# Optimization experiments

Hardware: AMD Instinct MI355X
Metric: run time of the kernel (lower is better)

Reference implementation:

```python
import jax, jax.numpy as jnp
import numpy as np

EPS = 1e-06  # slot-attention renorm epsilon
LN_EPS = 1e-05  # torch LayerNorm default
NUM_ITERS = 3


def layernorm(x, w, b):
    m = jnp.mean(x, axis=-1, keepdims=True)
    v = jnp.mean((x - m) ** 2, axis=-1, keepdims=True)
    return (x - m) * jax.lax.rsqrt(v + LN_EPS) * w + b


def setup_inputs() -> dict:
    key = jax.random.key(0)
    ks = jax.random.split(key, 16)
    B, N, D = 32, 4096, 512
    S, NS, H = 128, 8, 256
    def lin(k, out_f, in_f):
        return jax.random.normal(k, (out_f, in_f), jnp.float32) * (1.0 / np.sqrt(in_f))
    return {
        "inputs": jax.random.normal(ks[0], (B, N, D), jnp.float32),
        "slots_init": jax.random.normal(ks[1], (B, NS, S), jnp.float32),
        "ln_in_w": jnp.ones((D,), jnp.float32), "ln_in_b": jnp.zeros((D,), jnp.float32),
        "ln_slot_w": jnp.ones((S,), jnp.float32), "ln_slot_b": jnp.zeros((S,), jnp.float32),
        "ln_mlp_w": jnp.ones((S,), jnp.float32), "ln_mlp_b": jnp.zeros((S,), jnp.float32),
        "Wq": lin(ks[2], S, S), "Wk": lin(ks[3], S, D), "Wv": lin(ks[4], S, D),
        "gru_Wih": lin(ks[5], 3 * S, S), "gru_Whh": lin(ks[6], 3 * S, S),
        "gru_bih": jnp.zeros((3 * S,), jnp.float32), "gru_bhh": jnp.zeros((3 * S,), jnp.float32),
        "mlp_W1": lin(ks[7], H, S), "mlp_b1": jnp.zeros((H,), jnp.float32),
        "mlp_W2": lin(ks[8], S, H), "mlp_b2": jnp.zeros((S,), jnp.float32),
        "slots_mu": jax.random.normal(ks[9], (1, 1, S), jnp.float32) * 0.1,
        "slots_log_sigma": jax.random.normal(ks[10], (1, 1, S), jnp.float32) * 0.1,
    }


def gru_cell(x, h, Wih, Whh, bih, bhh):
    # PyTorch GRUCell math. x, h: [BS, S]
    S = h.shape[-1]
    gi = x @ Wih.T + bih
    gh = h @ Whh.T + bhh
    i_r, i_z, i_n = gi[:, :S], gi[:, S:2 * S], gi[:, 2 * S:]
    h_r, h_z, h_n = gh[:, :S], gh[:, S:2 * S], gh[:, 2 * S:]
    r = jax.nn.sigmoid(i_r + h_r)
    z = jax.nn.sigmoid(i_z + h_z)
    n = jnp.tanh(i_n + r * h_n)
    return (1.0 - z) * n + z * h


def reference(inputs, slots_init, ln_in_w, ln_in_b, ln_slot_w, ln_slot_b, ln_mlp_w, ln_mlp_b,
              Wq, Wk, Wv, gru_Wih, gru_Whh, gru_bih, gru_bhh,
              mlp_W1, mlp_b1, mlp_W2, mlp_b2, slots_mu, slots_log_sigma):
    B, N, D = inputs.shape
    NS, S = slots_init.shape[1], slots_init.shape[2]
    x = layernorm(inputs, ln_in_w, ln_in_b)
    k = jnp.einsum('bnd,sd->bns', x, Wk)  # [B,N,S]
    v = jnp.einsum('bnd,sd->bns', x, Wv)
    slots = slots_mu + jnp.exp(slots_log_sigma) * slots_init  # [B,NS,S]
    scale = S ** (-0.5)
    for _ in range(NUM_ITERS):
        slots_prev = slots
        q = jnp.einsum('bmd,sd->bms', layernorm(slots, ln_slot_w, ln_slot_b), Wq)  # [B,NS,S]
        attn_logits = scale * jnp.einsum('bns,bms->bnm', k, q)  # [B,N,NS]
        attn = jax.nn.softmax(attn_logits, axis=-1) + EPS
        attn = attn / jnp.sum(attn, axis=1, keepdims=True)  # normalize over inputs
        updates = jnp.einsum('bnm,bns->bms', attn, v)  # [B,NS,S]
        h = gru_cell(updates.reshape(B * NS, S), slots_prev.reshape(B * NS, S),
                     gru_Wih, gru_Whh, gru_bih, gru_bhh).reshape(B, NS, S)
        mlp_out = jnp.maximum(layernorm(h, ln_mlp_w, ln_mlp_b) @ mlp_W1.T + mlp_b1, 0.0) @ mlp_W2.T + mlp_b2
        slots = h + mlp_out
    return slots
```

## Files before the change

kernel.cpp:

```cpp
#include <hip/hip_runtime.h>

typedef __bf16 v8bf __attribute__((ext_vector_type(8)));
typedef __bf16 v4bf __attribute__((ext_vector_type(4)));
typedef float  v4f  __attribute__((ext_vector_type(4)));
typedef unsigned short u16;

#define LN_EPS_F 1e-5f
#define ATTN_EPS 1e-6f

static constexpr int Bsz = 32;
static constexpr int Nn  = 4096;
static constexpr int Dd  = 512;
static constexpr int Ss  = 128;
static constexpr int NSs = 8;
static constexpr int Hh  = 256;
static constexpr int MROWS = Bsz * Nn;

__global__ __launch_bounds__(256) void k_stats(const float* __restrict__ X,
                                               float2* __restrict__ stats) {
    const int wid  = threadIdx.x >> 6;
    const int lane = threadIdx.x & 63;
    const int row  = blockIdx.x * 4 + wid;
    const float4* xp = reinterpret_cast<const float4*>(X + (size_t)row * Dd) + lane * 2;
    float4 a = xp[0];
    float4 b = xp[1];
    float s  = a.x + a.y + a.z + a.w + b.x + b.y + b.z + b.w;
    float s2 = a.x*a.x + a.y*a.y + a.z*a.z + a.w*a.w
             + b.x*b.x + b.y*b.y + b.z*b.z + b.w*b.w;
#pragma unroll
    for (int off = 32; off > 0; off >>= 1) {
        s  += __shfl_xor(s, off);
        s2 += __shfl_xor(s2, off);
    }
    if (lane == 0) {
        float m = s * (1.0f / Dd);
        float v = s2 * (1.0f / Dd) - m * m;
        stats[row] = make_float2(m, rsqrtf(v + LN_EPS_F));
    }
}

__global__ __launch_bounds__(256) void k_prep(const float* __restrict__ Wk, const float* __restrict__ Wv,
                                              const float* __restrict__ ln_in_w, const float* __restrict__ ln_in_b,
                                              const float* __restrict__ slots_init, const float* __restrict__ mu,
                                              const float* __restrict__ lsig,
                                              u16* __restrict__ Wkvp, float* __restrict__ cb,
                                              float* __restrict__ slots) {
    const int bid = blockIdx.x;
    const int t = threadIdx.x;
    if (bid < 512) {
        int idx = bid * 256 + t;
        int n = idx >> 9, d = idx & 511;
        float w = (n < Ss) ? Wk[n * Dd + d] : Wv[(n - Ss) * Dd + d];
        w *= ln_in_w[d];
        __bf16 bv = (__bf16)w;
        Wkvp[idx] = __builtin_bit_cast(u16, bv);
    } else if (bid < 640) {
        int idx = (bid - 512) * 256 + t;
        int sidx = idx & (Ss - 1);
        slots[idx] = mu[sidx] + expf(lsig[sidx]) * slots_init[idx];
    } else {
        const float* wrow = (t < Ss) ? (Wk + t * Dd) : (Wv + (t - Ss) * Dd);
        float acc = 0.f;
        for (int d = 0; d < Dd; ++d) acc += ln_in_b[d] * wrow[d];
        cb[t] = acc;
    }
}

__global__ __launch_bounds__(256) void k_kvgemm(const float* __restrict__ X,
                                                const float2* __restrict__ stats,
                                                const u16* __restrict__ Wkvp,
                                                const float* __restrict__ cb,
                                                u16* __restrict__ kv) {
    __shared__ __bf16 As[64][72];
    __shared__ __bf16 Bs[256][72];
    const int t    = threadIdx.x;
    const int lane = t & 63;
    const int wid  = t >> 6;
    const size_t m0 = (size_t)blockIdx.x * 64;

    const int ar  = t >> 2;
    const int ac0 = (t & 3) * 16;
    const float2 st = stats[m0 + ar];
    const float* xrow = X + (m0 + ar) * Dd;
    const u16* wrow = Wkvp + t * Dd;

    const v4f vzero = {0.f, 0.f, 0.f, 0.f};
    v4f acc[4][4];
#pragma unroll
    for (int i = 0; i < 4; ++i)
#pragma unroll
        for (int j = 0; j < 4; ++j) acc[i][j] = vzero;

    const int g  = lane >> 4;
    const int lr = lane & 15;

    for (int kb = 0; kb < 8; ++kb) {
#pragma unroll
        for (int j = 0; j < 4; ++j) {
            float4 xv = *reinterpret_cast<const float4*>(xrow + kb * 64 + ac0 + j * 4);
            v4bf wv;
            wv[0] = (__bf16)((xv.x - st.x) * st.y);
            wv[1] = (__bf16)((xv.y - st.x) * st.y);
            wv[2] = (__bf16)((xv.z - st.x) * st.y);
            wv[3] = (__bf16)((xv.w - st.x) * st.y);
            *reinterpret_cast<v4bf*>(&As[ar][ac0 + j * 4]) = wv;
        }
#pragma unroll
        for (int p = 0; p < 8; ++p) {
            uint4 u = *reinterpret_cast<const uint4*>(wrow + kb * 64 + p * 8);
            *reinterpret_cast<uint4*>(&Bs[t][p * 8]) = u;
        }
        __syncthreads();
#pragma unroll
        for (int ks = 0; ks < 2; ++ks) {
            v8bf a[4], b[4];
#pragma unroll
            for (int mi = 0; mi < 4; ++mi)
                a[mi] = *reinterpret_cast<const v8bf*>(&As[mi * 16 + lr][ks * 32 + g * 8]);
#pragma unroll
            for (int ni = 0; ni < 4; ++ni)
                b[ni] = *reinterpret_cast<const v8bf*>(&Bs[wid * 64 + ni * 16 + lr][ks * 32 + g * 8]);
#pragma unroll
            for (int mi = 0; mi < 4; ++mi)
#pragma unroll
                for (int ni = 0; ni < 4; ++ni)
                    acc[mi][ni] = __builtin_amdgcn_mfma_f32_16x16x32_bf16(a[mi], b[ni], acc[mi][ni], 0, 0, 0);
        }
        __syncthreads();
    }
    float cbv[4];
#pragma unroll
    for (int ni = 0; ni < 4; ++ni) cbv[ni] = cb[wid * 64 + ni * 16 + lr];
#pragma unroll
    for (int mi = 0; mi < 4; ++mi)
#pragma unroll
        for (int ni = 0; ni < 4; ++ni)
#pragma unroll
            for (int j = 0; j < 4; ++j) {
                size_t mg = m0 + mi * 16 + g * 4 + j;
                int ng = wid * 64 + ni * 16 + lr;
                __bf16 bv = (__bf16)(acc[mi][ni][j] + cbv[ni]);
                kv[mg * 256 + ng] = __builtin_bit_cast(u16, bv);
            }
}

__global__ __launch_bounds__(128) void k_q(const float* __restrict__ slots,
                                           const float* __restrict__ lnw, const float* __restrict__ lnb,
                                           const float* __restrict__ Wq, float* __restrict__ q) {
    __shared__ float xs[128];
    __shared__ float red[4];
    const int t = threadIdx.x;
    const int bm = blockIdx.x;
    float x = slots[bm * 128 + t];
    float s = x, s2 = x * x;
#pragma unroll
    for (int off = 32; off > 0; off >>= 1) { s += __shfl_xor(s, off); s2 += __shfl_xor(s2, off); }
    const int wid = t >> 6, lane = t & 63;
    if (lane == 0) { red[wid * 2] = s; red[wid * 2 + 1] = s2; }
    __syncthreads();
    float S1 = red[0] + red[2], S2 = red[1] + red[3];
    float m = S1 * (1.f / 128.f);
    float rstd = rsqrtf(S2 * (1.f / 128.f) - m * m + LN_EPS_F);
    xs[t] = (x - m) * rstd * lnw[t] + lnb[t];
    __syncthreads();
    const float* wr = Wq + (size_t)t * 128;
    float acc = 0.f;
#pragma unroll 8
    for (int d = 0; d < 128; d += 4) {
        float4 w = *reinterpret_cast<const float4*>(wr + d);
        acc += w.x * xs[d] + w.y * xs[d + 1] + w.z * xs[d + 2] + w.w * xs[d + 3];
    }
    q[bm * 128 + t] = acc * 0.08838834764831845f;
}

__global__ __launch_bounds__(256) void k_attn(const u16* __restrict__ kv, const float* __restrict__ q,
                                              float* __restrict__ attn, float* __restrict__ colsum_part) {
    __shared__ float qs[8][128];
    __shared__ float colpart[4][8];
    const int b  = blockIdx.y;
    const int ch = blockIdx.x;
    const int t  = threadIdx.x;
    for (int i = t; i < NSs * Ss; i += 256) qs[i >> 7][i & 127] = q[b * (NSs * Ss) + i];
    __syncthreads();
    const int nl   = t >> 1;
    const int half = t & 1;
    const int n    = ch * 128 + nl;
    const u16* krow = kv + ((size_t)(b * Nn + n)) * 256 + half * 64;
    float acc[8] = {0.f, 0.f, 0.f, 0.f, 0.f, 0.f, 0.f, 0.f};
#pragma unroll
    for (int c = 0; c < 8; ++c) {
        v8bf kvv = *reinterpret_cast<const v8bf*>(krow + c * 8);
        float kf[8];
#pragma unroll
        for (int j = 0; j < 8; ++j) kf[j] = (float)kvv[j];
#pragma unroll
        for (int m = 0; m < 8; ++m) {
            const float* qrow = &qs[m][half * 64 + c * 8];
            float aa = 0.f;
#pragma unroll
            for (int j = 0; j < 8; ++j) aa += kf[j] * qrow[j];
            acc[m] += aa;
        }
    }
#pragma unroll
    for (int m = 0; m < 8; ++m) acc[m] += __shfl_xor(acc[m], 1);
    float mx = acc[0];
#pragma unroll
    for (int m = 1; m < 8; ++m) mx = fmaxf(mx, acc[m]);
    float e[8]; float ssum = 0.f;
#pragma unroll
    for (int m = 0; m < 8; ++m) { e[m] = __expf(acc[m] - mx); ssum += e[m]; }
    float inv = 1.0f / ssum;
    float a8[8];
#pragma unroll
    for (int m = 0; m < 8; ++m) a8[m] = e[m] * inv + ATTN_EPS;
    float4 outv = half ? make_float4(a8[4], a8[5], a8[6], a8[7])
                       : make_float4(a8[0], a8[1], a8[2], a8[3]);
    *reinterpret_cast<float4*>(attn + ((size_t)(b * Nn + n)) * 8 + half * 4) = outv;
    const int lane = t & 63, w = t >> 6;
#pragma unroll
    for (int m = 0; m < 8; ++m) {
        float v = a8[m];
#pragma unroll
        for (int off = 32; off > 0; off >>= 1) v += __shfl_xor(v, off);
        if (lane == 0) colpart[w][m] = v * 0.5f;
    }
    __syncthreads();
    if (t < 8)
        colsum_part[(b * 32 + ch) * 8 + t] =
            colpart[0][t] + colpart[1][t] + colpart[2][t] + colpart[3][t];
}

__global__ __launch_bounds__(256) void k_upd(const u16* __restrict__ kv, const float* __restrict__ attn,
                                             float* __restrict__ upd_part) {
    __shared__ float at[128][8];
    __shared__ __bf16 vt[128][128];
    const int b  = blockIdx.y;
    const int ch = blockIdx.x;
    const int t  = threadIdx.x;
    {
        float4 v = *reinterpret_cast<const float4*>(attn + ((size_t)(b * Nn + ch * 128)) * 8 + t * 4);
        *reinterpret_cast<float4*>(&at[t >> 1][(t & 1) * 4]) = v;
    }
#pragma unroll
    for (int p = 0; p < 8; ++p) {
        int r = p * 16 + (t >> 4);
        int c = (t & 15) * 8;
        uint4 u = *reinterpret_cast<const uint4*>(kv + ((size_t)(b * Nn + ch * 128 + r)) * 256 + 128 + c);
        *reinterpret_cast<uint4*>(&vt[r][c]) = u;
    }
    __syncthreads();
    const int m  = t >> 5;
    const int s0 = (t & 31) * 4;
    float a0 = 0.f, a1 = 0.f, a2 = 0.f, a3 = 0.f;
#pragma unroll 4
    for (int n = 0; n < 128; ++n) {
        float a = at[n][m];
        v4bf vv = *reinterpret_cast<const v4bf*>(&vt[n][s0]);
        a0 += a * (float)vv[0];
        a1 += a * (float)vv[1];
        a2 += a * (float)vv[2];
        a3 += a * (float)vv[3];
    }
    *reinterpret_cast<float4*>(upd_part + ((size_t)(b * 32 + ch) * 8 + m) * 128 + s0) =
        make_float4(a0, a1, a2, a3);
}

__global__ __launch_bounds__(128) void k_finish(const float* __restrict__ upd_part,
                                                const float* __restrict__ colsum_part,
                                                const float* __restrict__ slots_in,
                                                const float* __restrict__ Wih, const float* __restrict__ Whh,
                                                const float* __restrict__ bih, const float* __restrict__ bhh,
                                                const float* __restrict__ lnw, const float* __restrict__ lnb,
                                                const float* __restrict__ W1, const float* __restrict__ b1,
                                                const float* __restrict__ W2, const float* __restrict__ b2,
                                                float* __restrict__ slots_out) {
    __shared__ float us[128], sp[128], hnorm[128], act[256];
    __shared__ float red[4];
    __shared__ float csum_sh;
    const int t  = threadIdx.x;
    const int bm = blockIdx.x;
    const int b = bm >> 3, m = bm & 7;
    if (t < 64) {
        float v = (t < 32) ? colsum_part[(b * 32 + t) * 8 + m] : 0.f;
#pragma unroll
        for (int off = 32; off > 0; off >>= 1) v += __shfl_xor(v, off);
        if (t == 0) csum_sh = v;
    }
    float u = 0.f;
    for (int chk = 0; chk < 32; ++chk)
        u += upd_part[((size_t)(b * 32 + chk) * 8 + m) * 128 + t];
    float h0 = slots_in[bm * 128 + t];
    sp[t] = h0;
    __syncthreads();
    u *= (1.0f / csum_sh);
    us[t] = u;
    __syncthreads();
    float gir = bih[t], giz = bih[Ss + t], gin = bih[2 * Ss + t];
    float ghr = bhh[t], ghz = bhh[Ss + t], ghn = bhh[2 * Ss + t];
#pragma unroll 4
    for (int d = 0; d < Ss; d += 4) {
        float u0 = us[d], u1 = us[d + 1], u2 = us[d + 2], u3 = us[d + 3];
        float p0 = sp[d], p1 = sp[d + 1], p2 = sp[d + 2], p3 = sp[d + 3];
        float4 w;
        w = *reinterpret_cast<const float4*>(Wih + (size_t)t * Ss + d);
        gir += w.x * u0 + w.y * u1 + w.z * u2 + w.w * u3;
        w = *reinterpret_cast<const float4*>(Wih + (size_t)(Ss + t) * Ss + d);
        giz += w.x * u0 + w.y * u1 + w.z * u2 + w.w * u3;
        w = *reinterpret_cast<const float4*>(Wih + (size_t)(2 * Ss + t) * Ss + d);
        gin += w.x * u0 + w.y * u1 + w.z * u2 + w.w * u3;
        w = *reinterpret_cast<const float4*>(Whh + (size_t)t * Ss + d);
        ghr += w.x * p0 + w.y * p1 + w.z * p2 + w.w * p3;
        w = *reinterpret_cast<const float4*>(Whh + (size_t)(Ss + t) * Ss + d);
        ghz += w.x * p0 + w.y * p1 + w.z * p2 + w.w * p3;
        w = *reinterpret_cast<const float4*>(Whh + (size_t)(2 * Ss + t) * Ss + d);
        ghn += w.x * p0 + w.y * p1 + w.z * p2 + w.w * p3;
    }
    float r  = 1.f / (1.f + __expf(-(gir + ghr)));
    float z  = 1.f / (1.f + __expf(-(giz + ghz)));
    float nn = tanhf(gin + r * ghn);
    float h  = (1.f - z) * nn + z * h0;
    float s = h, s2 = h * h;
#pragma unroll
    for (int off = 32; off > 0; off >>= 1) { s += __shfl_xor(s, off); s2 += __shfl_xor(s2, off); }
    const int lane = t & 63, w2 = t >> 6;
    if (lane == 0) { red[w2 * 2] = s; red[w2 * 2 + 1] = s2; }
    __syncthreads();
    float S1 = red[0] + red[2], S2 = red[1] + red[3];
    float mean = S1 * (1.f / Ss);
    float rstd = rsqrtf(S2 * (1.f / Ss) - mean * mean + LN_EPS_F);
    hnorm[t] = (h - mean) * rstd * lnw[t] + lnb[t];
    __syncthreads();
    float a1 = b1[t], a2 = b1[Ss + t];
#pragma unroll 4
    for (int d = 0; d < Ss; d += 4) {
        float h0_ = hnorm[d], h1_ = hnorm[d + 1], h2_ = hnorm[d + 2], h3_ = hnorm[d + 3];
        float4 w1v = *reinterpret_cast<const float4*>(W1 + (size_t)t * Ss + d);
        float4 w2v = *reinterpret_cast<const float4*>(W1 + (size_t)(Ss + t) * Ss + d);
        a1 += w1v.x * h0_ + w1v.y * h1_ + w1v.z * h2_ + w1v.w * h3_;
        a2 += w2v.x * h0_ + w2v.y * h1_ + w2v.z * h2_ + w2v.w * h3_;
    }
    act[t] = fmaxf(a1, 0.f);
    act[Ss + t] = fmaxf(a2, 0.f);
    __syncthreads();
    float o = b2[t];
#pragma unroll 4
    for (int j = 0; j < Hh; j += 4) {
        float4 wv = *reinterpret_cast<const float4*>(W2 + (size_t)t * Hh + j);
        o += wv.x * act[j] + wv.y * act[j + 1] + wv.z * act[j + 2] + wv.w * act[j + 3];
    }
    slots_out[bm * 128 + t] = h + o;
}

extern "C" void kernel_launch(void* const* d_in, const int* in_sizes, int n_in,
                              void* d_out, int out_size, void* d_ws, size_t ws_size,
                              hipStream_t stream) {
    const float* X          = (const float*)d_in[0];
    const float* slots_init = (const float*)d_in[1];
    const float* ln_in_w    = (const float*)d_in[2];
    const float* ln_in_b    = (const float*)d_in[3];
    const float* ln_slot_w  = (const float*)d_in[4];
    const float* ln_slot_b  = (const float*)d_in[5];
    const float* ln_mlp_w   = (const float*)d_in[6];
    const float* ln_mlp_b   = (const float*)d_in[7];
    const float* Wq         = (const float*)d_in[8];
    const float* Wk         = (const float*)d_in[9];
    const float* Wv         = (const float*)d_in[10];
    const float* gWih       = (const float*)d_in[11];
    const float* gWhh       = (const float*)d_in[12];
    const float* gbih       = (const float*)d_in[13];
    const float* gbhh       = (const float*)d_in[14];
    const float* W1         = (const float*)d_in[15];
    const float* b1         = (const float*)d_in[16];
    const float* W2         = (const float*)d_in[17];
    const float* b2         = (const float*)d_in[18];
    const float* mu         = (const float*)d_in[19];
    const float* lsig       = (const float*)d_in[20];

    char* p = (char*)d_ws;
    float2* stats       = (float2*)p; p += (size_t)MROWS * sizeof(float2);
    u16*    Wkvp        = (u16*)p;    p += (size_t)256 * 512 * sizeof(u16);
    float*  cb          = (float*)p;  p += 256 * sizeof(float);
    float*  slots       = (float*)p;  p += 32 * 8 * 128 * sizeof(float);
    float*  qbuf        = (float*)p;  p += 32 * 8 * 128 * sizeof(float);
    float*  colsum_part = (float*)p;  p += 32 * 32 * 8 * sizeof(float);
    float*  upd_part    = (float*)p;  p += (size_t)32 * 32 * 8 * 128 * sizeof(float);
    float*  attn        = (float*)p;  p += (size_t)MROWS * 8 * sizeof(float);
    u16*    kv          = (u16*)p;    p += (size_t)MROWS * 256 * sizeof(u16);

    k_stats<<<MROWS / 4, 256, 0, stream>>>(X, stats);
    k_prep<<<641, 256, 0, stream>>>(Wk, Wv, ln_in_w, ln_in_b, slots_init, mu, lsig,
                                    Wkvp, cb, slots);
    k_kvgemm<<<MROWS / 64, 256, 0, stream>>>(X, stats, Wkvp, cb, kv);

    for (int it = 0; it < 3; ++it) {
        k_q<<<256, 128, 0, stream>>>(slots, ln_slot_w, ln_slot_b, Wq, qbuf);
        k_attn<<<dim3(32, 32), 256, 0, stream>>>(kv, qbuf, attn, colsum_part);
        k_upd<<<dim3(32, 32), 256, 0, stream>>>(kv, attn, upd_part);
        k_finish<<<256, 128, 0, stream>>>(upd_part, colsum_part, slots,
                                          gWih, gWhh, gbih, gbhh,
                                          ln_mlp_w, ln_mlp_b, W1, b1, W2, b2,
                                          (it == 2) ? (float*)d_out : slots);
    }
}
```

Before: 370.1 us.

## Fuse LayerNorm stats into KV GEMM, merge attn/update and finish/q kernels

Removes the separate row-stats pass by applying input LayerNorm algebraically after the GEMM, using per-column weight sums and row mean/rstd accumulated while the tile is loaded. The B tile now goes through direct global-to-LDS loads into an XOR-swizzled layout. The attention and update kernels are fused so the attn matrix never goes to global memory, and the q projection is folded into the finish kernel. The aim is to cut a full 256MB read of X plus the attn round-trip and several launches, at the cost of bf16 rounding on raw X before centering, which may lose precision.

```diff
diff --git a/kernel.cpp b/kernel.cpp
--- a/kernel.cpp
+++ b/kernel.cpp
@@ -16,27 +16,10 @@
 static constexpr int Hh  = 256;
 static constexpr int MROWS = Bsz * Nn;
 
-__global__ __launch_bounds__(256) void k_stats(const float* __restrict__ X,
-                                               float2* __restrict__ stats) {
-    const int wid  = threadIdx.x >> 6;
-    const int lane = threadIdx.x & 63;
-    const int row  = blockIdx.x * 4 + wid;
-    const float4* xp = reinterpret_cast<const float4*>(X + (size_t)row * Dd) + lane * 2;
-    float4 a = xp[0];
-    float4 b = xp[1];
-    float s  = a.x + a.y + a.z + a.w + b.x + b.y + b.z + b.w;
-    float s2 = a.x*a.x + a.y*a.y + a.z*a.z + a.w*a.w
-             + b.x*b.x + b.y*b.y + b.z*b.z + b.w*b.w;
-#pragma unroll
-    for (int off = 32; off > 0; off >>= 1) {
-        s  += __shfl_xor(s, off);
-        s2 += __shfl_xor(s2, off);
-    }
-    if (lane == 0) {
-        float m = s * (1.0f / Dd);
-        float v = s2 * (1.0f / Dd) - m * m;
-        stats[row] = make_float2(m, rsqrtf(v + LN_EPS_F));
-    }
+__device__ __forceinline__ void load_lds16(const void* g, void* l) {
+    __builtin_amdgcn_global_load_lds(
+        (const __attribute__((address_space(1))) void*)g,
+        (__attribute__((address_space(3))) void*)l, 16, 0, 0);
 }
 
 __global__ __launch_bounds__(256) void k_prep(const float* __restrict__ Wk, const float* __restrict__ Wv,
@@ -44,7 +27,7 @@
                                               const float* __restrict__ slots_init, const float* __restrict__ mu,
                                               const float* __restrict__ lsig,
                                               u16* __restrict__ Wkvp, float* __restrict__ cb,
-                                              float* __restrict__ slots) {
+                                              float* __restrict__ Scol, float* __restrict__ slots) {
     const int bid = blockIdx.x;
     const int t = threadIdx.x;
     if (bid < 512) {
@@ -60,19 +43,26 @@
         slots[idx] = mu[sidx] + expf(lsig[sidx]) * slots_init[idx];
     } else {
         const float* wrow = (t < Ss) ? (Wk + t * Dd) : (Wv + (t - Ss) * Dd);
-        float acc = 0.f;
-        for (int d = 0; d < Dd; ++d) acc += ln_in_b[d] * wrow[d];
-        cb[t] = acc;
+        float accb = 0.f, accs = 0.f;
+        for (int d = 0; d < Dd; ++d) {
+            float w  = wrow[d];
+            float wb = (float)(__bf16)(w * ln_in_w[d]);
+            accs += wb;
+            accb += ln_in_b[d] * w;
+        }
+        cb[t]   = accb;
+        Scol[t] = accs;
     }
 }
 
 __global__ __launch_bounds__(256) void k_kvgemm(const float* __restrict__ X,
-                                                const float2* __restrict__ stats,
                                                 const u16* __restrict__ Wkvp,
                                                 const float* __restrict__ cb,
+                                                const float* __restrict__ Scol,
                                                 u16* __restrict__ kv) {
     __shared__ __bf16 As[64][72];
-    __shared__ __bf16 Bs[256][72];
+    __shared__ __bf16 Bs[256 * 64];
+    __shared__ float2 stats_sh[64];
     const int t    = threadIdx.x;
     const int lane = t & 63;
     const int wid  = t >> 6;
@@ -80,9 +70,11 @@
 
     const int ar  = t >> 2;
     const int ac0 = (t & 3) * 16;
-    const float2 st = stats[m0 + ar];
     const float* xrow = X + (m0 + ar) * Dd;
-    const u16* wrow = Wkvp + t * Dd;
+
+    const int sub  = lane >> 3;
+    const int scol = ((lane & 7) ^ sub) * 8;
+    const u16* bsrc = Wkvp + (size_t)(wid * 64 + sub) * Dd + scol;
 
     const v4f vzero = {0.f, 0.f, 0.f, 0.f};
     v4f acc[4][4];
@@ -93,22 +85,22 @@
 
     const int g  = lane >> 4;
     const int lr = lane & 15;
+    float s1 = 0.f, s2 = 0.f;
 
     for (int kb = 0; kb < 8; ++kb) {
+#pragma unroll
+        for (int p = 0; p < 8; ++p)
+            load_lds16(bsrc + (size_t)p * 8 * Dd + kb * 64,
+                       &Bs[(wid * 64 + p * 8) * 64]);
 #pragma unroll
         for (int j = 0; j < 4; ++j) {
             float4 xv = *reinterpret_cast<const float4*>(xrow + kb * 64 + ac0 + j * 4);
+            s1 += xv.x + xv.y + xv.z + xv.w;
+            s2 += xv.x * xv.x + xv.y * xv.y + xv.z * xv.z + xv.w * xv.w;
             v4bf wv;
-            wv[0] = (__bf16)((xv.x - st.x) * st.y);
-            wv[1] = (__bf16)((xv.y - st.x) * st.y);
-            wv[2] = (__bf16)((xv.z - st.x) * st.y);
-            wv[3] = (__bf16)((xv.w - st.x) * st.y);
+            wv[0] = (__bf16)xv.x; wv[1] = (__bf16)xv.y;
+            wv[2] = (__bf16)xv.z; wv[3] = (__bf16)xv.w;
             *reinterpret_cast<v4bf*>(&As[ar][ac0 + j * 4]) = wv;
-        }
-#pragma unroll
-        for (int p = 0; p < 8; ++p) {
-            uint4 u = *reinterpret_cast<const uint4*>(wrow + kb * 64 + p * 8);
-            *reinterpret_cast<uint4*>(&Bs[t][p * 8]) = u;
         }
         __syncthreads();
 #pragma unroll
@@ -118,8 +110,11 @@
             for (int mi = 0; mi < 4; ++mi)
                 a[mi] = *reinterpret_cast<const v8bf*>(&As[mi * 16 + lr][ks * 32 + g * 8]);
 #pragma unroll
-            for (int ni = 0; ni < 4; ++ni)
-                b[ni] = *reinterpret_cast<const v8bf*>(&Bs[wid * 64 + ni * 16 + lr][ks * 32 + g * 8]);
+            for (int ni = 0; ni < 4; ++ni) {
+                int r = wid * 64 + ni * 16 + lr;
+                b[ni] = *reinterpret_cast<const v8bf*>(
+                    &Bs[r * 64 + ((ks * 32 + g * 8) ^ ((lr & 7) * 8))]);
+            }
 #pragma unroll
             for (int mi = 0; mi < 4; ++mi)
 #pragma unroll
@@ -128,20 +123,35 @@
         }
         __syncthreads();
     }
-    float cbv[4];
-#pragma unroll
-    for (int ni = 0; ni < 4; ++ni) cbv[ni] = cb[wid * 64 + ni * 16 + lr];
+    s1 += __shfl_xor(s1, 1); s1 += __shfl_xor(s1, 2);
+    s2 += __shfl_xor(s2, 1); s2 += __shfl_xor(s2, 2);
+    if ((t & 3) == 0) {
+        float m = s1 * (1.f / Dd);
+        float v = s2 * (1.f / Dd) - m * m;
+        stats_sh[ar] = make_float2(m, rsqrtf(v + LN_EPS_F));
+    }
+    __syncthreads();
+    float Sn[4], cbv[4];
+#pragma unroll
+    for (int ni = 0; ni < 4; ++ni) {
+        int ng = wid * 64 + ni * 16 + lr;
+        Sn[ni]  = Scol[ng];
+        cbv[ni] = cb[ng];
+    }
 #pragma unroll
     for (int mi = 0; mi < 4; ++mi)
 #pragma unroll
-        for (int ni = 0; ni < 4; ++ni)
-#pragma unroll
-            for (int j = 0; j < 4; ++j) {
-                size_t mg = m0 + mi * 16 + g * 4 + j;
+        for (int j = 0; j < 4; ++j) {
+            float2 st = stats_sh[mi * 16 + g * 4 + j];
+            size_t mg = m0 + mi * 16 + g * 4 + j;
+#pragma unroll
+            for (int ni = 0; ni < 4; ++ni) {
                 int ng = wid * 64 + ni * 16 + lr;
-                __bf16 bv = (__bf16)(acc[mi][ni][j] + cbv[ni]);
+                float val = st.y * (acc[mi][ni][j] - st.x * Sn[ni]) + cbv[ni];
+                __bf16 bv = (__bf16)val;
                 kv[mg * 256 + ng] = __builtin_bit_cast(u16, bv);
             }
+        }
 }
 
 __global__ __launch_bounds__(128) void k_q(const float* __restrict__ slots,
@@ -173,19 +183,31 @@
     q[bm * 128 + t] = acc * 0.08838834764831845f;
 }
 
-__global__ __launch_bounds__(256) void k_attn(const u16* __restrict__ kv, const float* __restrict__ q,
-                                              float* __restrict__ attn, float* __restrict__ colsum_part) {
-    __shared__ float qs[8][128];
+__global__ __launch_bounds__(256) void k_attnupd(const u16* __restrict__ kv, const float* __restrict__ q,
+                                                 float* __restrict__ upd_part, float* __restrict__ colsum_part) {
+    __shared__ float qs[8 * 128];
+    __shared__ float at[128][8];
+    __shared__ __bf16 vt[128][128];
     __shared__ float colpart[4][8];
     const int b  = blockIdx.y;
     const int ch = blockIdx.x;
     const int t  = threadIdx.x;
-    for (int i = t; i < NSs * Ss; i += 256) qs[i >> 7][i & 127] = q[b * (NSs * Ss) + i];
-    __syncthreads();
+    const int lane = t & 63, wv = t >> 6;
+    *reinterpret_cast<float4*>(&qs[t * 4]) = *reinterpret_cast<const float4*>(&q[b * 1024 + t * 4]);
+    __syncthreads();
+    {
+        const int rsub = lane >> 4;
+        const int csub = (lane & 15) * 8;
+#pragma unroll
+        for (int p = 0; p < 8; ++p) {
+            int row = wv * 32 + p * 4;
+            const u16* src = kv + ((size_t)(b * Nn + ch * 128 + row + rsub)) * 256 + 128 + csub;
+            load_lds16(src, &vt[row][0]);
+        }
+    }
     const int nl   = t >> 1;
     const int half = t & 1;
-    const int n    = ch * 128 + nl;
-    const u16* krow = kv + ((size_t)(b * Nn + n)) * 256 + half * 64;
+    const u16* krow = kv + ((size_t)(b * Nn + ch * 128 + nl)) * 256 + half * 64;
     float acc[8] = {0.f, 0.f, 0.f, 0.f, 0.f, 0.f, 0.f, 0.f};
 #pragma unroll
     for (int c = 0; c < 8; ++c) {
@@ -195,7 +217,7 @@
         for (int j = 0; j < 8; ++j) kf[j] = (float)kvv[j];
 #pragma unroll
         for (int m = 0; m < 8; ++m) {
-            const float* qrow = &qs[m][half * 64 + c * 8];
+            const float* qrow = &qs[m * 128 + half * 64 + c * 8];
             float aa = 0.f;
 #pragma unroll
             for (int j = 0; j < 8; ++j) aa += kf[j] * qrow[j];
@@ -214,67 +236,46 @@
     float a8[8];
 #pragma unroll
     for (int m = 0; m < 8; ++m) a8[m] = e[m] * inv + ATTN_EPS;
-    float4 outv = half ? make_float4(a8[4], a8[5], a8[6], a8[7])
-                       : make_float4(a8[0], a8[1], a8[2], a8[3]);
-    *reinterpret_cast<float4*>(attn + ((size_t)(b * Nn + n)) * 8 + half * 4) = outv;
-    const int lane = t & 63, w = t >> 6;
+    *reinterpret_cast<float4*>(&at[nl][half * 4]) =
+        make_float4(a8[half * 4], a8[half * 4 + 1], a8[half * 4 + 2], a8[half * 4 + 3]);
 #pragma unroll
     for (int m = 0; m < 8; ++m) {
         float v = a8[m];
 #pragma unroll
         for (int off = 32; off > 0; off >>= 1) v += __shfl_xor(v, off);
-        if (lane == 0) colpart[w][m] = v * 0.5f;
-    }
-    __syncthreads();
-    if (t < 8)
-        colsum_part[(b * 32 + ch) * 8 + t] =
-            colpart[0][t] + colpart[1][t] + colpart[2][t] + colpart[3][t];
-}
-
-__global__ __launch_bounds__(256) void k_upd(const u16* __restrict__ kv, const float* __restrict__ attn,
-                                             float* __restrict__ upd_part) {
-    __shared__ float at[128][8];
-    __shared__ __bf16 vt[128][128];
-    const int b  = blockIdx.y;
-    const int ch = blockIdx.x;
-    const int t  = threadIdx.x;
-    {
-        float4 v = *reinterpret_cast<const float4*>(attn + ((size_t)(b * Nn + ch * 128)) * 8 + t * 4);
-        *reinterpret_cast<float4*>(&at[t >> 1][(t & 1) * 4]) = v;
-    }
-#pragma unroll
-    for (int p = 0; p < 8; ++p) {
-        int r = p * 16 + (t >> 4);
-        int c = (t & 15) * 8;
-        uint4 u = *reinterpret_cast<const uint4*>(kv + ((size_t)(b * Nn + ch * 128 + r)) * 256 + 128 + c);
-        *reinterpret_cast<uint4*>(&vt[r][c]) = u;
-    }
-    __syncthreads();
-    const int m  = t >> 5;
+        if (lane == 0) colpart[wv][m] = v * 0.5f;
+    }
+    __syncthreads();
+    const int m2 = t >> 5;
     const int s0 = (t & 31) * 4;
     float a0 = 0.f, a1 = 0.f, a2 = 0.f, a3 = 0.f;
 #pragma unroll 4
     for (int n = 0; n < 128; ++n) {
-        float a = at[n][m];
-        v4bf vv = *reinterpret_cast<const v4bf*>(&vt[n][s0]);
-        a0 += a * (float)vv[0];
-        a1 += a * (float)vv[1];
-        a2 += a * (float)vv[2];
-        a3 += a * (float)vv[3];
-    }
-    *reinterpret_cast<float4*>(upd_part + ((size_t)(b * 32 + ch) * 8 + m) * 128 + s0) =
+        float a = at[n][m2];
+        v4bf vvv = *reinterpret_cast<const v4bf*>(&vt[n][s0]);
+        a0 += a * (float)vvv[0];
+        a1 += a * (float)vvv[1];
+        a2 += a * (float)vvv[2];
+        a3 += a * (float)vvv[3];
+    }
+    *reinterpret_cast<float4*>(upd_part + ((size_t)(b * 32 + ch) * 8 + m2) * 128 + s0) =
         make_float4(a0, a1, a2, a3);
-}
-
-__global__ __launch_bounds__(128) void k_finish(const float* __restrict__ upd_part,
-                                                const float* __restrict__ colsum_part,
-                                                const float* __restrict__ slots_in,
-                                                const float* __restrict__ Wih, const float* __restrict__ Whh,
-                                                const float* __restrict__ bih, const float* __restrict__ bhh,
-                                                const float* __restrict__ lnw, const float* __restrict__ lnb,
-                                                const float* __restrict__ W1, const float* __restrict__ b1,
-                                                const float* __restrict__ W2, const float* __restrict__ b2,
-                                                float* __restrict__ slots_out) {
+    if (t < 8)
+        colsum_part[(b * 32 + ch) * 8 + t] =
+            colpart[0][t] + colpart[1][t] + colpart[2][t] + colpart[3][t];
+}
+
+__global__ __launch_bounds__(128) void k_finishq(const float* __restrict__ upd_part,
+                                                 const float* __restrict__ colsum_part,
+                                                 const float* __restrict__ slots_in,
+                                                 const float* __restrict__ Wih, const float* __restrict__ Whh,
+                                                 const float* __restrict__ bih, const float* __restrict__ bhh,
+                                                 const float* __restrict__ lnw, const float* __restrict__ lnb,
+                                                 const float* __restrict__ W1, const float* __restrict__ b1,
+                                                 const float* __restrict__ W2, const float* __restrict__ b2,
+                                                 const float* __restrict__ lnsw, const float* __restrict__ lnsb,
+                                                 const float* __restrict__ Wq,
+                                                 float* __restrict__ slots_out, float* __restrict__ qout) {
     __shared__ float us[128], sp[128], hnorm[128], act[256];
     __shared__ float red[4];
     __shared__ float csum_sh;
@@ -349,7 +350,26 @@
         float4 wv = *reinterpret_cast<const float4*>(W2 + (size_t)t * Hh + j);
         o += wv.x * act[j] + wv.y * act[j + 1] + wv.z * act[j + 2] + wv.w * act[j + 3];
     }
-    slots_out[bm * 128 + t] = h + o;
+    float snew = h + o;
+    slots_out[bm * 128 + t] = snew;
+    float ss1 = snew, ss2 = snew * snew;
+#pragma unroll
+    for (int off = 32; off > 0; off >>= 1) { ss1 += __shfl_xor(ss1, off); ss2 += __shfl_xor(ss2, off); }
+    if (lane == 0) { red[w2 * 2] = ss1; red[w2 * 2 + 1] = ss2; }
+    __syncthreads();
+    float T1 = red[0] + red[2], T2 = red[1] + red[3];
+    float m2 = T1 * (1.f / Ss);
+    float rstd2 = rsqrtf(T2 * (1.f / Ss) - m2 * m2 + LN_EPS_F);
+    hnorm[t] = (snew - m2) * rstd2 * lnsw[t] + lnsb[t];
+    __syncthreads();
+    const float* wr = Wq + (size_t)t * 128;
+    float qa = 0.f;
+#pragma unroll 8
+    for (int d = 0; d < 128; d += 4) {
+        float4 w = *reinterpret_cast<const float4*>(wr + d);
+        qa += w.x * hnorm[d] + w.y * hnorm[d + 1] + w.z * hnorm[d + 2] + w.w * hnorm[d + 3];
+    }
+    qout[bm * 128 + t] = qa * 0.08838834764831845f;
 }
 
 extern "C" void kernel_launch(void* const* d_in, const int* in_sizes, int n_in,
@@ -378,28 +398,26 @@
     const float* lsig       = (const float*)d_in[20];
 
     char* p = (char*)d_ws;
-    float2* stats       = (float2*)p; p += (size_t)MROWS * sizeof(float2);
     u16*    Wkvp        = (u16*)p;    p += (size_t)256 * 512 * sizeof(u16);
     float*  cb          = (float*)p;  p += 256 * sizeof(float);
+    float*  Scol        = (float*)p;  p += 256 * sizeof(float);
     float*  slots       = (float*)p;  p += 32 * 8 * 128 * sizeof(float);
     float*  qbuf        = (float*)p;  p += 32 * 8 * 128 * sizeof(float);
     float*  colsum_part = (float*)p;  p += 32 * 32 * 8 * sizeof(float);
     float*  upd_part    = (float*)p;  p += (size_t)32 * 32 * 8 * 128 * sizeof(float);
-    float*  attn        = (float*)p;  p += (size_t)MROWS * 8 * sizeof(float);
     u16*    kv          = (u16*)p;    p += (size_t)MROWS * 256 * sizeof(u16);
 
-    k_stats<<<MROWS / 4, 256, 0, stream>>>(X, stats);
     k_prep<<<641, 256, 0, stream>>>(Wk, Wv, ln_in_w, ln_in_b, slots_init, mu, lsig,
-                                    Wkvp, cb, slots);
-    k_kvgemm<<<MROWS / 64, 256, 0, stream>>>(X, stats, Wkvp, cb, kv);
+                                    Wkvp, cb, Scol, slots);
+    k_kvgemm<<<MROWS / 64, 256, 0, stream>>>(X, Wkvp, cb, Scol, kv);
+    k_q<<<256, 128, 0, stream>>>(slots, ln_slot_w, ln_slot_b, Wq, qbuf);
 
     for (int it = 0; it < 3; ++it) {
-        k_q<<<256, 128, 0, stream>>>(slots, ln_slot_w, ln_slot_b, Wq, qbuf);
-        k_attn<<<dim3(32, 32), 256, 0, stream>>>(kv, qbuf, attn, colsum_part);
-        k_upd<<<dim3(32, 32), 256, 0, stream>>>(kv, attn, upd_part);
-        k_finish<<<256, 128, 0, stream>>>(upd_part, colsum_part, slots,
-                                          gWih, gWhh, gbih, gbhh,
-                                          ln_mlp_w, ln_mlp_b, W1, b1, W2, b2,
-                                          (it == 2) ? (float*)d_out : slots);
-    }
-}
+        k_attnupd<<<dim3(32, 32), 256, 0, stream>>>(kv, qbuf, upd_part, colsum_part);
+        k_finishq<<<256, 128, 0, stream>>>(upd_part, colsum_part, slots,
+                                           gWih, gWhh, gbih, gbhh,
+                                           ln_mlp_w, ln_mlp_b, W1, b1, W2, b2,
+                                           ln_slot_w, ln_slot_b, Wq,
+                                           (it == 2) ? (float*)d_out : slots, qbuf);
+    }
+}
```

Result: faster. 308.3 us (-16.7%).
